# Performance work log

Measured on AMD Instinct MI355X. Metric: run time of the kernel, lower is better.

The kernel has to match this reference:

```python
import jax, jax.numpy as jnp
import numpy as np

H = 181  # hidden size

def setup_inputs() -> dict:
    key = jax.random.key(0)
    ks = jax.random.split(key, 7)
    B, T, I, C = 1024, 1024, 1, 10
    x = jax.random.normal(ks[0], (B, T, I), dtype=jnp.float32)
    w_ih = jax.random.normal(ks[1], (3 * H, I), dtype=jnp.float32) * 0.5
    w_hh = jax.random.normal(ks[2], (3 * H, H), dtype=jnp.float32) * (1.0 / np.sqrt(H))
    b_ih = jax.random.normal(ks[3], (3 * H,), dtype=jnp.float32) * 0.1
    b_hh = jax.random.normal(ks[4], (3 * H,), dtype=jnp.float32) * 0.1
    w_fc = jax.random.normal(ks[5], (C, H), dtype=jnp.float32) * (1.0 / np.sqrt(H))
    b_fc = jax.random.normal(ks[6], (C,), dtype=jnp.float32) * 0.1
    return {"x": x, "w_ih": w_ih, "w_hh": w_hh, "b_ih": b_ih, "b_hh": b_hh,
            "w_fc": w_fc, "b_fc": b_fc}

def _gru_last_hidden(x, w_ih, w_hh, b_ih, b_hh):
    # x: [B, T, I]. Precompute input-side gate pre-activations for all steps.
    B = x.shape[0]
    gi = jnp.einsum('bti,gi->btg', x, w_ih) + b_ih  # [B, T, 3H]
    gi = jnp.swapaxes(gi, 0, 1)                     # [T, B, 3H] for scan
    h0 = jnp.zeros((B, H), dtype=x.dtype)

    def step(h, gi_t):
        gh = h @ w_hh.T + b_hh                      # [B, 3H]
        r = jax.nn.sigmoid(gi_t[:, :H] + gh[:, :H])
        z = jax.nn.sigmoid(gi_t[:, H:2 * H] + gh[:, H:2 * H])
        n = jnp.tanh(gi_t[:, 2 * H:] + r * gh[:, 2 * H:])
        h_new = (1.0 - z) * n + z * h
        return h_new, None

    h_last, _ = jax.lax.scan(step, h0, gi)
    return h_last  # [B, H]

def reference(x, w_ih, w_hh, b_ih, b_hh, w_fc, b_fc):
    h_last = _gru_last_hidden(x, w_ih, w_hh, b_ih, b_hh)
    logits = h_last @ w_fc.T + b_fc  # [B, num_classes]
    return logits
```

## Files before the change

kernel.cpp:

```cpp
#include <hip/hip_runtime.h>

#define H 181
#define T_LEN 1024
#define BB 4
#define NBLK 256
#define NTHR 768
#define KT3 3
#define FRAGB 1024
#define PST 192
#define XSTR 1027

typedef __attribute__((ext_vector_type(4))) int   intx4;

#define LOG2E 1.4426950408889634f
#define SCH_C  1064992506.0f
#define SCH_LO 897220352.0f
#define SCH_HI 1182433024.0f

__device__ __forceinline__ float exp2_fast(float g) {
    float s = fmaf(g, 8388608.0f, SCH_C);
    s = fminf(fmaxf(s, SCH_LO), SCH_HI);
    return __uint_as_float((unsigned)s);
}
__device__ __forceinline__ float rcpf(float x)   { return __builtin_amdgcn_rcpf(x); }
__device__ __forceinline__ float exp2hw(float x) { return __builtin_amdgcn_exp2f(x); }

__launch_bounds__(NTHR, 3)
__global__ void gru_i8(const float* __restrict__ x,
                       const float* __restrict__ w_ih,
                       const float* __restrict__ w_hh,
                       const float* __restrict__ b_ih,
                       const float* __restrict__ b_hh,
                       const float* __restrict__ w_fc,
                       const float* __restrict__ b_fc,
                       float* __restrict__ out) {
    __shared__ __align__(16) char  hfr_s[2 * KT3 * FRAGB];
    __shared__ __align__(16) float x_s[BB * XSTR];
    __shared__ float wsc_s[3 * PST];
    __shared__ volatile char pad_s[57344];

    const int tid  = threadIdx.x;
    const int jt   = tid >> 6;
    const int lane = tid & 63;
    const int col  = lane & 15;
    const int q    = lane >> 4;
    const int b0   = blockIdx.x * BB;
    if (tid == 0) pad_s[0] = 0;

    const int  mu = jt * 16 + col;
    const bool mv = (mu < H);
    intx4 afr[3][KT3];
    #pragma unroll
    for (int g = 0; g < 3; ++g) {
        const float* wrow = w_hh + (size_t)(g * H + (mv ? mu : 0)) * H;
        float rm = 0.0f;
        if (mv) for (int k = 0; k < H; ++k) rm = fmaxf(rm, fabsf(wrow[k]));
        float s    = (rm > 1e-30f) ? rm * (1.0f / 127.0f) : 1.0f;
        float invs = 1.0f / s;
        #pragma unroll
        for (int kt = 0; kt < KT3; ++kt) {
            union { signed char c[16]; intx4 v; } uu;
            #pragma unroll
            for (int e = 0; e < 16; ++e) {
                int k = kt * 64 + q * 16 + e;
                float v = (mv && k < H) ? wrow[k] * invs : 0.0f;
                v = fminf(fmaxf(rintf(v), -127.0f), 127.0f);
                uu.c[e] = (signed char)(int)v;
            }
            afr[g][kt] = uu.v;
        }
        if (q == 0) wsc_s[g * PST + mu] = s;
    }

    for (int i = tid; i < BB * T_LEN; i += NTHR) {
        int bb = i >> 10, t = i & 1023;
        x_s[bb * XSTR + t] = x[(size_t)b0 * T_LEN + i];
    }
    {
        int* hz = (int*)hfr_s;
        for (int i = tid; i < 2 * KT3 * FRAGB / 4; i += NTHR) hz[i] = 0;
    }
    __syncthreads();

    const int  rr4 = (col >> 2) & 3;
    const int  b   = col & 3;
    const int  u   = jt * 16 + q * 4 + rr4;
    const bool jv  = (u < H);
    const float dqR = -LOG2E * wsc_s[0 * PST + u] * (1.0f / 127.0f);
    const float dqZ = -LOG2E * wsc_s[1 * PST + u] * (1.0f / 127.0f);
    const float dqN =  2.0f * LOG2E * wsc_s[2 * PST + u] * (1.0f / 127.0f);
    const float baseR = jv ? -LOG2E * (b_ih[u] + b_hh[u])             : 0.0f;
    const float baseZ = jv ? -LOG2E * (b_ih[H + u] + b_hh[H + u])     : 0.0f;
    const float baseN = jv ?  2.0f * LOG2E * b_hh[2 * H + u]          : 0.0f;
    const float wrS = jv ? -LOG2E * w_ih[u]                : 0.0f;
    const float wzS = jv ? -LOG2E * w_ih[H + u]            : 0.0f;
    const float wnS = jv ?  2.0f * LOG2E * w_ih[2 * H + u] : 0.0f;
    const float bnI = jv ?  2.0f * LOG2E * b_ih[2 * H + u] : 0.0f;
    const int woffB = (jt >> 2) * FRAGB + (((jt & 3) * 16 + b) * 16) + q * 4;
    const int rbase = lane * 16;

    float h = 0.0f;

    auto step = [&](const char* rb, char* wb, int t) {
        intx4 bf[KT3];
        #pragma unroll
        for (int kt = 0; kt < KT3; ++kt)
            bf[kt] = *(const intx4*)(rb + kt * FRAGB + rbase);
        intx4 aR = {0,0,0,0}, aZ = {0,0,0,0}, aN = {0,0,0,0};
        #pragma unroll
        for (int kt = 0; kt < KT3; ++kt) {
            aR = __builtin_amdgcn_mfma_i32_16x16x64_i8(afr[0][kt], bf[kt], aR, 0, 0, 0);
            aZ = __builtin_amdgcn_mfma_i32_16x16x64_i8(afr[1][kt], bf[kt], aZ, 0, 0, 0);
            aN = __builtin_amdgcn_mfma_i32_16x16x64_i8(afr[2][kt], bf[kt], aN, 0, 0, 0);
        }

        int vR = aR[0], vZ = aZ[0], vN = aN[0];
        vR = __builtin_amdgcn_update_dpp(vR, aR[1], 0x114, 0xF, 0x2, false);
        vR = __builtin_amdgcn_update_dpp(vR, aR[2], 0x118, 0xF, 0x4, false);
        vR = __builtin_amdgcn_update_dpp(vR, aR[3], 0x11C, 0xF, 0x8, false);
        vZ = __builtin_amdgcn_update_dpp(vZ, aZ[1], 0x114, 0xF, 0x2, false);
        vZ = __builtin_amdgcn_update_dpp(vZ, aZ[2], 0x118, 0xF, 0x4, false);
        vZ = __builtin_amdgcn_update_dpp(vZ, aZ[3], 0x11C, 0xF, 0x8, false);
        vN = __builtin_amdgcn_update_dpp(vN, aN[1], 0x114, 0xF, 0x2, false);
        vN = __builtin_amdgcn_update_dpp(vN, aN[2], 0x118, 0xF, 0x4, false);
        vN = __builtin_amdgcn_update_dpp(vN, aN[3], 0x11C, 0xF, 0x8, false);

        float pR = fmaf((float)vR, dqR, baseR);
        float pZ = fmaf((float)vZ, dqZ, baseZ);
        float pN = fmaf((float)vN, dqN, baseN);
        float xv = x_s[b * XSTR + t];

        float er = exp2_fast(fmaf(xv, wrS, pR));
        float ez = exp2hw(fminf(fmaf(xv, wzS, pZ), 14.0f));
        float dR = 1.0f + er, dZ = 1.0f + ez;
        float qq = rcpf(dR * dZ);
        float rr = qq * dZ, zz = qq * dR;
        float gn = fmaf(rr, pN, fmaf(xv, wnS, bnI));
        float en = exp2hw(fminf(gn, 30.0f));
        float nn = fmaf(-2.0f, rcpf(1.0f + en), 1.0f);
        h = fmaf(zz, h - nn, nn);

        int iq = (int)rintf(h * 127.0f);
        int hq = jv ? (iq & 255) : 0;
        int t1 = __builtin_amdgcn_update_dpp(0, hq, 0x104, 0xF, 0xF, true);
        int t2 = __builtin_amdgcn_update_dpp(0, hq, 0x108, 0xF, 0xF, true);
        int t3 = __builtin_amdgcn_update_dpp(0, hq, 0x10C, 0xF, 0xF, true);
        int p01 = __builtin_amdgcn_perm(t1, hq, 0x05010400);
        int p23 = __builtin_amdgcn_perm(t3, t2, 0x05010400);
        int pk  = __builtin_amdgcn_perm(p23, p01, 0x05040100);
        if (rr4 == 0)
            *(int*)(wb + woffB) = pk;
        __syncthreads();
    };

    char* buf0 = hfr_s;
    char* buf1 = hfr_s + KT3 * FRAGB;
    for (int t = 0; t < T_LEN; t += 2) {
        step(buf0, buf1, t);
        step(buf1, buf0, t + 1);
    }

    __syncthreads();
    if (u < PST) x_s[b * PST + u] = h;
    __syncthreads();
    if (tid < BB * 10) {
        int bb = tid / 10, c = tid % 10;
        float acc = b_fc[c];
        for (int k = 0; k < H; ++k)
            acc = fmaf(x_s[bb * PST + k], w_fc[c * H + k], acc);
        out[(b0 + bb) * 10 + c] = acc;
    }
}

extern "C" void kernel_launch(void* const* d_in, const int* in_sizes, int n_in,
                              void* d_out, int out_size, void* d_ws, size_t ws_size,
                              hipStream_t stream) {
    const float* x    = (const float*)d_in[0];
    const float* w_ih = (const float*)d_in[1];
    const float* w_hh = (const float*)d_in[2];
    const float* b_ih = (const float*)d_in[3];
    const float* b_hh = (const float*)d_in[4];
    const float* w_fc = (const float*)d_in[5];
    const float* b_fc = (const float*)d_in[6];
    float* out = (float*)d_out;

    gru_i8<<<NBLK, NTHR, 0, stream>>>(x, w_ih, w_hh, b_ih, b_hh, w_fc, b_fc, out);
}
```

Before: 715.0 us.

## Halve batch per block, give each wave two gate tiles, drop LDS padding

Each block now handles 2 batch rows with 6 waves instead of 4 rows with 12 waves, and 512 blocks are launched instead of 256. Each wave now covers two 16-unit row tiles, running 18 int8 MFMAs per step and merging the accumulator lanes from both tiles with DPP. The LDS padding array, which capped how many blocks fit per CU, is removed, so more blocks can be resident at once. The trade is more MFMA and DPP work per wave per step, in exchange for fewer waves meeting at each per-step barrier and more independent blocks to hide latency.

```diff
diff --git a/kernel.cpp b/kernel.cpp
--- a/kernel.cpp
+++ b/kernel.cpp
@@ -2,15 +2,15 @@
 
 #define H 181
 #define T_LEN 1024
-#define BB 4
-#define NBLK 256
-#define NTHR 768
+#define BB 2
+#define NBLK 512
+#define NTHR 384
 #define KT3 3
 #define FRAGB 1024
 #define PST 192
 #define XSTR 1027
 
-typedef __attribute__((ext_vector_type(4))) int   intx4;
+typedef __attribute__((ext_vector_type(4))) int intx4;
 
 #define LOG2E 1.4426950408889634f
 #define SCH_C  1064992506.0f
@@ -37,7 +37,6 @@
     __shared__ __align__(16) char  hfr_s[2 * KT3 * FRAGB];
     __shared__ __align__(16) float x_s[BB * XSTR];
     __shared__ float wsc_s[3 * PST];
-    __shared__ volatile char pad_s[57344];
 
     const int tid  = threadIdx.x;
     const int jt   = tid >> 6;
@@ -45,31 +44,33 @@
     const int col  = lane & 15;
     const int q    = lane >> 4;
     const int b0   = blockIdx.x * BB;
-    if (tid == 0) pad_s[0] = 0;
-
-    const int  mu = jt * 16 + col;
-    const bool mv = (mu < H);
-    intx4 afr[3][KT3];
+
+    intx4 afr[2][3][KT3];
     #pragma unroll
-    for (int g = 0; g < 3; ++g) {
-        const float* wrow = w_hh + (size_t)(g * H + (mv ? mu : 0)) * H;
-        float rm = 0.0f;
-        if (mv) for (int k = 0; k < H; ++k) rm = fmaxf(rm, fabsf(wrow[k]));
-        float s    = (rm > 1e-30f) ? rm * (1.0f / 127.0f) : 1.0f;
-        float invs = 1.0f / s;
-        #pragma unroll
-        for (int kt = 0; kt < KT3; ++kt) {
-            union { signed char c[16]; intx4 v; } uu;
+    for (int tt = 0; tt < 2; ++tt) {
+        const int  mu = (2 * jt + tt) * 16 + col;
+        const bool mv = (mu < H);
+        #pragma unroll
+        for (int g = 0; g < 3; ++g) {
+            const float* wrow = w_hh + (size_t)(g * H + (mv ? mu : 0)) * H;
+            float rm = 0.0f;
+            if (mv) for (int k = 0; k < H; ++k) rm = fmaxf(rm, fabsf(wrow[k]));
+            float s    = (rm > 1e-30f) ? rm * (1.0f / 127.0f) : 1.0f;
+            float invs = 1.0f / s;
             #pragma unroll
-            for (int e = 0; e < 16; ++e) {
-                int k = kt * 64 + q * 16 + e;
-                float v = (mv && k < H) ? wrow[k] * invs : 0.0f;
-                v = fminf(fmaxf(rintf(v), -127.0f), 127.0f);
-                uu.c[e] = (signed char)(int)v;
+            for (int kt = 0; kt < KT3; ++kt) {
+                union { signed char c[16]; intx4 v; } uu;
+                #pragma unroll
+                for (int e = 0; e < 16; ++e) {
+                    int k = kt * 64 + q * 16 + e;
+                    float v = (mv && k < H) ? wrow[k] * invs : 0.0f;
+                    v = fminf(fmaxf(rintf(v), -127.0f), 127.0f);
+                    uu.c[e] = (signed char)(int)v;
+                }
+                afr[tt][g][kt] = uu.v;
             }
-            afr[g][kt] = uu.v;
+            if (q == 0) wsc_s[g * PST + mu] = s;
         }
-        if (q == 0) wsc_s[g * PST + mu] = s;
     }
 
     for (int i = tid; i < BB * T_LEN; i += NTHR) {
@@ -82,9 +83,10 @@
     }
     __syncthreads();
 
-    const int  rr4 = (col >> 2) & 3;
-    const int  b   = col & 3;
-    const int  u   = jt * 16 + q * 4 + rr4;
+    const int  rr4 = (lane >> 2) & 3;
+    const int  tau = (lane >> 1) & 1;
+    const int  b   = lane & 1;
+    const int  u   = (2 * jt + tau) * 16 + q * 4 + rr4;
     const bool jv  = (u < H);
     const float dqR = -LOG2E * wsc_s[0 * PST + u] * (1.0f / 127.0f);
     const float dqZ = -LOG2E * wsc_s[1 * PST + u] * (1.0f / 127.0f);
@@ -96,7 +98,8 @@
     const float wzS = jv ? -LOG2E * w_ih[H + u]            : 0.0f;
     const float wnS = jv ?  2.0f * LOG2E * w_ih[2 * H + u] : 0.0f;
     const float bnI = jv ?  2.0f * LOG2E * b_ih[2 * H + u] : 0.0f;
-    const int woffB = (jt >> 2) * FRAGB + (((jt & 3) * 16 + b) * 16) + q * 4;
+    const int u0    = (2 * jt + tau) * 16 + q * 4;
+    const int woffB = (u0 >> 6) * FRAGB + (((u0 >> 4) & 3) * 16 + b) * 16 + (u0 & 15);
     const int rbase = lane * 16;
 
     float h = 0.0f;
@@ -106,28 +109,38 @@
         #pragma unroll
         for (int kt = 0; kt < KT3; ++kt)
             bf[kt] = *(const intx4*)(rb + kt * FRAGB + rbase);
-        intx4 aR = {0,0,0,0}, aZ = {0,0,0,0}, aN = {0,0,0,0};
-        #pragma unroll
-        for (int kt = 0; kt < KT3; ++kt) {
-            aR = __builtin_amdgcn_mfma_i32_16x16x64_i8(afr[0][kt], bf[kt], aR, 0, 0, 0);
-            aZ = __builtin_amdgcn_mfma_i32_16x16x64_i8(afr[1][kt], bf[kt], aZ, 0, 0, 0);
-            aN = __builtin_amdgcn_mfma_i32_16x16x64_i8(afr[2][kt], bf[kt], aN, 0, 0, 0);
+        intx4 ac[2][3];
+        #pragma unroll
+        for (int tt = 0; tt < 2; ++tt)
+            #pragma unroll
+            for (int g = 0; g < 3; ++g)
+                ac[tt][g] = (intx4){0, 0, 0, 0};
+        #pragma unroll
+        for (int kt = 0; kt < KT3; ++kt)
+            #pragma unroll
+            for (int tt = 0; tt < 2; ++tt) {
+                ac[tt][0] = __builtin_amdgcn_mfma_i32_16x16x64_i8(afr[tt][0][kt], bf[kt], ac[tt][0], 0, 0, 0);
+                ac[tt][1] = __builtin_amdgcn_mfma_i32_16x16x64_i8(afr[tt][1][kt], bf[kt], ac[tt][1], 0, 0, 0);
+                ac[tt][2] = __builtin_amdgcn_mfma_i32_16x16x64_i8(afr[tt][2][kt], bf[kt], ac[tt][2], 0, 0, 0);
+            }
+
+        int v3[3];
+        #pragma unroll
+        for (int g = 0; g < 3; ++g) {
+            int v = ac[0][g][0];
+            v = __builtin_amdgcn_update_dpp(v, ac[0][g][1], 0x114, 0xF, 0x2, false);
+            v = __builtin_amdgcn_update_dpp(v, ac[0][g][2], 0x118, 0xF, 0x4, false);
+            v = __builtin_amdgcn_update_dpp(v, ac[0][g][3], 0x11C, 0xF, 0x8, false);
+            v = __builtin_amdgcn_update_dpp(v, ac[1][g][0], 0x112, 0xF, 0x1, false);
+            v = __builtin_amdgcn_update_dpp(v, ac[1][g][1], 0x116, 0xF, 0x2, false);
+            v = __builtin_amdgcn_update_dpp(v, ac[1][g][2], 0x11A, 0xF, 0x4, false);
+            v = __builtin_amdgcn_update_dpp(v, ac[1][g][3], 0x11E, 0xF, 0x8, false);
+            v3[g] = v;
         }
 
-        int vR = aR[0], vZ = aZ[0], vN = aN[0];
-        vR = __builtin_amdgcn_update_dpp(vR, aR[1], 0x114, 0xF, 0x2, false);
-        vR = __builtin_amdgcn_update_dpp(vR, aR[2], 0x118, 0xF, 0x4, false);
-        vR = __builtin_amdgcn_update_dpp(vR, aR[3], 0x11C, 0xF, 0x8, false);
-        vZ = __builtin_amdgcn_update_dpp(vZ, aZ[1], 0x114, 0xF, 0x2, false);
-        vZ = __builtin_amdgcn_update_dpp(vZ, aZ[2], 0x118, 0xF, 0x4, false);
-        vZ = __builtin_amdgcn_update_dpp(vZ, aZ[3], 0x11C, 0xF, 0x8, false);
-        vN = __builtin_amdgcn_update_dpp(vN, aN[1], 0x114, 0xF, 0x2, false);
-        vN = __builtin_amdgcn_update_dpp(vN, aN[2], 0x118, 0xF, 0x4, false);
-        vN = __builtin_amdgcn_update_dpp(vN, aN[3], 0x11C, 0xF, 0x8, false);
-
-        float pR = fmaf((float)vR, dqR, baseR);
-        float pZ = fmaf((float)vZ, dqZ, baseZ);
-        float pN = fmaf((float)vN, dqN, baseN);
+        float pR = fmaf((float)v3[0], dqR, baseR);
+        float pZ = fmaf((float)v3[1], dqZ, baseZ);
+        float pN = fmaf((float)v3[2], dqN, baseN);
         float xv = x_s[b * XSTR + t];
 
         float er = exp2_fast(fmaf(xv, wrS, pR));
@@ -161,7 +174,7 @@
     }
 
     __syncthreads();
-    if (u < PST) x_s[b * PST + u] = h;
+    x_s[b * PST + u] = h;
     __syncthreads();
     if (tid < BB * 10) {
         int bb = tid / 10, c = tid % 10;
```

After: 1.449 ms. 103% more time.
